# Kernel optimization log

Hardware: AMD Instinct MI355X
Metric: run time of the kernel (lower is better)

The kernel has to match this reference:

```python
import jax, jax.numpy as jnp
import numpy as np

N, C, D = 131072, 512, 3


def setup_inputs() -> dict:
    key = jax.random.key(0)
    kx, kmu = jax.random.split(key)
    X = jax.random.normal(kx, (N, D), dtype=jnp.float32)
    mu = jax.random.normal(kmu, (C, D), dtype=jnp.float32)
    w = jnp.zeros((C,), dtype=jnp.float32)
    # sigma as in __init__: r = sqrt(sum of per-dim unbiased variances of mu0)
    r = jnp.sqrt(jnp.var(mu, axis=0, ddof=1).sum())
    sigma = (0.1 * (r / C ** (1.0 / D))).astype(jnp.float32)
    return {"X": X, "mu": mu, "w": w, "sigma": sigma}


def reference(X, mu, w, sigma):
    # One EM step of a uniform-covariance GMM (EM_step_pytorch).
    n, d = X.shape
    # pairwise squared distances [N, C]
    D2_nc = ((X[:, None, :] - mu[None, :, :]) ** 2).sum(-1)
    # log-responsibilities (E-step), softmax over components
    lgamma_nc = jax.nn.log_softmax(w[None, :] - D2_nc / (2.0 * sigma ** 2), axis=1)
    gamma_nc = jnp.exp(lgamma_nc)
    # M-step: centroids (softmax over points, per component)
    mu_new = jax.nn.softmax(lgamma_nc, axis=0).T @ X  # [C, D]
    # M-step: component scores
    h_c = jax.nn.logsumexp(lgamma_nc, axis=0)  # [C]
    w_new = h_c - h_c.mean()
    # M-step: uniform std
    sigma_new = jnp.sqrt((gamma_nc * D2_nc).sum() / (d * n))
    # EM values: expected targets and free energy
    Y = gamma_nc @ mu_new  # [N, D]
    logpi_c = w_new - jax.nn.logsumexp(w_new)
    Cfe = (gamma_nc * (
        ((mu_new ** 2).sum(-1)[None, :] - (Y ** 2).sum(-1)[:, None]) / (2.0 * sigma_new ** 2)
        + d * jnp.log(sigma_new)
        - logpi_c[None, :]
        + lgamma_nc
    )).sum()
    return Y, Cfe
```

## Files before the change

### kernel.cpp

```cpp
#include <hip/hip_runtime.h>
#include <cfloat>
#include <cmath>

#define NPTS 131072
#define NC   512
#define NREP 4

#define PM4_OFF  0
#define PQ4_OFF  2048
#define ST4_OFF  4096
#define MISC_OFF 12288

__device__ __forceinline__ float waveSum(float v) {
#pragma unroll
  for (int off = 32; off > 0; off >>= 1) v += __shfl_down(v, off, 64);
  return v;
}
__device__ __forceinline__ float waveMax(float v) {
#pragma unroll
  for (int off = 32; off > 0; off >>= 1) v = fmaxf(v, __shfl_down(v, off, 64));
  return v;
}

__global__ __launch_bounds__(512) void k_prep(
    const float* __restrict__ mu, const float* __restrict__ w,
    const float* __restrict__ sigma, float4* __restrict__ pm,
    float* __restrict__ ST, float* __restrict__ misc) {
  const int t = threadIdx.x;
  const float sg = sigma[0];
  const float inv2s2 = 1.0f / (2.0f * sg * sg);
  const float m0 = mu[3 * t], m1 = mu[3 * t + 1], m2 = mu[3 * t + 2];
  pm[t] = make_float4(2.0f * inv2s2 * m0, 2.0f * inv2s2 * m1, 2.0f * inv2s2 * m2,
                      w[t] - (m0 * m0 + m1 * m1 + m2 * m2) * inv2s2);
#pragma unroll
  for (int r = 0; r < NREP * 4; ++r) ST[r * 512 + t] = 0.f;
  if (t < 8) misc[t] = 0.f;
}

__global__ __launch_bounds__(512, 8) void k_estep(
    const float* __restrict__ X, const float4* __restrict__ pm,
    float* __restrict__ ST, float* __restrict__ misc,
    float* __restrict__ out) {
  __shared__ float4 s_pt[128];
  __shared__ float2 s_ms[4][128];
  __shared__ float  s_red[8];
  __shared__ float  s_red2[8];

  const int t = threadIdx.x;
  const int p = t & 127;
  const int ch = __builtin_amdgcn_readfirstlane(t >> 7);
  const int n = blockIdx.x * 128 + p;
  const float x0 = X[3 * n], x1 = X[3 * n + 1], x2 = X[3 * n + 2];

  const float4* __restrict__ pmc = pm + ch * 128;
  float ma = -FLT_MAX, mb = -FLT_MAX, mc = -FLT_MAX, md = -FLT_MAX;
#pragma unroll 4
  for (int i = 0; i < 128; i += 4) {
    float4 a = pmc[i], b = pmc[i + 1], c = pmc[i + 2], d = pmc[i + 3];
    ma = fmaxf(ma, fmaf(a.x, x0, fmaf(a.y, x1, fmaf(a.z, x2, a.w))));
    mb = fmaxf(mb, fmaf(b.x, x0, fmaf(b.y, x1, fmaf(b.z, x2, b.w))));
    mc = fmaxf(mc, fmaf(c.x, x0, fmaf(c.y, x1, fmaf(c.z, x2, c.w))));
    md = fmaxf(md, fmaf(d.x, x0, fmaf(d.y, x1, fmaf(d.z, x2, d.w))));
  }
  const float m = fmaxf(fmaxf(ma, mb), fmaxf(mc, md));
  float sa = 0.f, sb = 0.f, sc = 0.f, sd = 0.f;
#pragma unroll 4
  for (int i = 0; i < 128; i += 4) {
    float4 a = pmc[i], b = pmc[i + 1], c = pmc[i + 2], d = pmc[i + 3];
    sa += __expf(fmaf(a.x, x0, fmaf(a.y, x1, fmaf(a.z, x2, a.w))) - m);
    sb += __expf(fmaf(b.x, x0, fmaf(b.y, x1, fmaf(b.z, x2, b.w))) - m);
    sc += __expf(fmaf(c.x, x0, fmaf(c.y, x1, fmaf(c.z, x2, c.w))) - m);
    sd += __expf(fmaf(d.x, x0, fmaf(d.y, x1, fmaf(d.z, x2, d.w))) - m);
  }
  s_ms[ch][p] = make_float2(m, (sa + sb) + (sc + sd));
  __syncthreads();

  if (t < 128) {
    float2 q0 = s_ms[0][t], q1 = s_ms[1][t], q2 = s_ms[2][t], q3 = s_ms[3][t];
    float M = fmaxf(fmaxf(q0.x, q1.x), fmaxf(q2.x, q3.x));
    float SS = q0.y * __expf(q0.x - M) + q1.y * __expf(q1.x - M) +
               q2.y * __expf(q2.x - M) + q3.y * __expf(q3.x - M);
    float z = M + __logf(SS);
    s_pt[t] = make_float4(x0, x1, x2, z);
    out[3 * n] = z;
  }
  __syncthreads();

  const float4 pc = pm[t];
  float Sg = 0.f, Tx = 0.f, Ty = 0.f, Tz = 0.f, La = 0.f;
#pragma unroll 4
  for (int i = 0; i < 128; ++i) {
    float4 pt = s_pt[i];
    float l = fmaf(pc.x, pt.x, fmaf(pc.y, pt.y, fmaf(pc.z, pt.z, pc.w)));
    float d = l - pt.w;
    float g = __expf(d);
    Sg += g;
    Tx = fmaf(g, pt.x, Tx);
    Ty = fmaf(g, pt.y, Ty);
    Tz = fmaf(g, pt.z, Tz);
    La = fmaf(g, d, La);
  }
  float* st = ST + (((blockIdx.x & (NREP - 1)) * 512 + t) << 2);
  atomicAdd(st + 0, Tx);
  atomicAdd(st + 1, Ty);
  atomicAdd(st + 2, Tz);
  atomicAdd(st + 3, Sg);

  float xx = (t < 128) ? (x0 * x0 + x1 * x1 + x2 * x2) : 0.f;
  float rx = waveSum(xx);
  float rl = waveSum(La);
  if ((t & 63) == 0) { s_red[t >> 6] = rx; s_red2[t >> 6] = rl; }
  __syncthreads();
  if (t == 0) {
    float vx = 0.f, vl = 0.f;
#pragma unroll
    for (int i = 0; i < 8; ++i) { vx += s_red[i]; vl += s_red2[i]; }
    atomicAdd(&misc[0], vx);
    atomicAdd(&misc[3], vl);
  }
}

__global__ __launch_bounds__(512) void k_mstep(
    const float* __restrict__ mu, const float4* __restrict__ ST4,
    float4* __restrict__ pq, float* __restrict__ misc,
    float* __restrict__ out) {
  __shared__ float s_red[8];
  __shared__ float s_red2[8];
  __shared__ float s_bc[4];
  const int t = threadIdx.x;

  float Tx = 0.f, Ty = 0.f, Tz = 0.f, S = 0.f;
#pragma unroll
  for (int r = 0; r < NREP; ++r) {
    float4 v = ST4[r * 512 + t];
    Tx += v.x; Ty += v.y; Tz += v.z; S += v.w;
  }
  const float Sc = fmaxf(S, 1e-30f);
  const float h = __logf(Sc);
  const float m0 = Tx / Sc, m1 = Ty / Sc, m2 = Tz / Sc;

  const float o0 = mu[3 * t], o1 = mu[3 * t + 1], o2 = mu[3 * t + 2];
  const float gdp = S * (o0 * o0 + o1 * o1 + o2 * o2)
                    - 2.0f * (o0 * Tx + o1 * Ty + o2 * Tz);

  float hm = waveMax(h);
  if ((t & 63) == 0) s_red[t >> 6] = hm;
  __syncthreads();
  if (t == 0) {
    float v = s_red[0];
    for (int i = 1; i < 8; ++i) v = fmaxf(v, s_red[i]);
    s_bc[0] = v;
  }
  __syncthreads();
  const float hM = s_bc[0];

  float es = waveSum(__expf(h - hM));
  float gs = waveSum(gdp);
  if ((t & 63) == 0) { s_red[t >> 6] = es; s_red2[t >> 6] = gs; }
  __syncthreads();
  if (t == 0) {
    float esum = 0.f, gsum = 0.f;
    for (int i = 0; i < 8; ++i) { esum += s_red[i]; gsum += s_red2[i]; }
    s_bc[1] = hM + __logf(esum);
    const float gd = fmaxf(misc[0] + gsum, 1e-20f);
    const float sn2 = gd * (1.0f / (3.0f * (float)NPTS));
    s_bc[2] = 1.0f / (2.0f * sn2);
    s_bc[3] = 1.5f * __logf(sn2);
  }
  __syncthreads();

  const float inv2s2n = s_bc[2];
  const float logpi = h - s_bc[1];
  const float A = (m0 * m0 + m1 * m1 + m2 * m2) * inv2s2n - logpi;
  pq[t] = make_float4(m0, m1, m2, A);

  float ca = waveSum(S * A);
  if ((t & 63) == 0) s_red[t >> 6] = ca;
  __syncthreads();
  if (t == 0) {
    float v = 0.f;
    for (int i = 0; i < 8; ++i) v += s_red[i];
    out[NPTS * 3] = v + misc[3] + (float)NPTS * s_bc[3];
    misc[1] = inv2s2n;
  }
}

__global__ __launch_bounds__(512, 8) void k_final(
    const float* __restrict__ X, const float4* __restrict__ pm,
    const float4* __restrict__ pq, const float* __restrict__ misc,
    float* __restrict__ out) {
  __shared__ float4 s_y[4][128];
  __shared__ float  s_red[8];

  const int t = threadIdx.x;
  const int p = t & 127;
  const int ch = __builtin_amdgcn_readfirstlane(t >> 7);
  const int n = blockIdx.x * 128 + p;
  const float x0 = X[3 * n], x1 = X[3 * n + 1], x2 = X[3 * n + 2];
  const float z = out[3 * n];
  const float inv2s2n = misc[1];

  const float4* __restrict__ pmc = pm + ch * 128;
  const float4* __restrict__ pqc = pq + ch * 128;
  float y0 = 0.f, y1 = 0.f, y2 = 0.f;
#pragma unroll 4
  for (int i = 0; i < 128; ++i) {
    float4 pp = pmc[i];
    float4 qq = pqc[i];
    float l = fmaf(pp.x, x0, fmaf(pp.y, x1, fmaf(pp.z, x2, pp.w))) - z;
    float g = __expf(l);
    y0 = fmaf(g, qq.x, y0);
    y1 = fmaf(g, qq.y, y1);
    y2 = fmaf(g, qq.z, y2);
  }
  s_y[ch][p] = make_float4(y0, y1, y2, 0.f);
  __syncthreads();

  float cfe = 0.f;
  if (t < 128) {
    float4 a0 = s_y[0][t], a1 = s_y[1][t], a2 = s_y[2][t], a3 = s_y[3][t];
    float Y0 = (a0.x + a1.x) + (a2.x + a3.x);
    float Y1 = (a0.y + a1.y) + (a2.y + a3.y);
    float Y2 = (a0.z + a1.z) + (a2.z + a3.z);
    cfe = -(Y0 * Y0 + Y1 * Y1 + Y2 * Y2) * inv2s2n;
    out[3 * n] = Y0;
    out[3 * n + 1] = Y1;
    out[3 * n + 2] = Y2;
  }
  float r = waveSum(cfe);
  if ((t & 63) == 0) s_red[t >> 6] = r;
  __syncthreads();
  if (t == 0) {
    float v = 0.f;
#pragma unroll
    for (int i = 0; i < 8; ++i) v += s_red[i];
    atomicAdd(&out[NPTS * 3], v);
  }
}

extern "C" void kernel_launch(void* const* d_in, const int* in_sizes, int n_in,
                              void* d_out, int out_size, void* d_ws, size_t ws_size,
                              hipStream_t stream) {
  const float* X = (const float*)d_in[0];
  const float* mu = (const float*)d_in[1];
  const float* w = (const float*)d_in[2];
  const float* sigma = (const float*)d_in[3];
  float* out = (float*)d_out;
  float* ws = (float*)d_ws;

  float4* pm = (float4*)(ws + PM4_OFF);
  float4* pq = (float4*)(ws + PQ4_OFF);
  float* ST = ws + ST4_OFF;
  float* misc = ws + MISC_OFF;

  k_prep<<<1, 512, 0, stream>>>(mu, w, sigma, pm, ST, misc);
  k_estep<<<NPTS / 128, 512, 0, stream>>>(X, pm, ST, misc, out);
  k_mstep<<<1, 512, 0, stream>>>(mu, (const float4*)ST, pq, misc, out);
  k_final<<<NPTS / 128, 512, 0, stream>>>(X, pm, pq, misc, out);
}
```

Baseline: 143.1 us.

## Restructure E-step in log2 domain and skip negligible responsibilities

Moves all logits into base-2 so exp2f and log2f can be used, and skips exp and accumulation work for components whose logit is more than 34 (log2 units) below the per-point max. The E-step is reorganised around 64 points per block with 8 component chunks. Logits are cached in a register array, and the entropy term is computed per point instead of per component. The point-to-component sums are scattered through LDS atomics before the global atomic flush. The final pass stages the pm/pq tables in LDS and applies the same cutoff. Gains depend on how sparse the responsibilities are. The risks are divergence, LDS atomic contention, higher register pressure, and a small approximation from dropping terms below the threshold.

```diff
diff --git a/kernel.cpp b/kernel.cpp
--- a/kernel.cpp
+++ b/kernel.cpp
@@ -5,6 +5,9 @@
 #define NPTS 131072
 #define NC   512
 #define NREP 4
+#define L2E  1.4426950408889634f
+#define LN2  0.6931471805599453f
+#define CUT  34.0f
 
 #define PM4_OFF  0
 #define PQ4_OFF  2048
@@ -28,95 +31,110 @@
     float* __restrict__ ST, float* __restrict__ misc) {
   const int t = threadIdx.x;
   const float sg = sigma[0];
-  const float inv2s2 = 1.0f / (2.0f * sg * sg);
+  const float k2 = L2E / (2.0f * sg * sg);
   const float m0 = mu[3 * t], m1 = mu[3 * t + 1], m2 = mu[3 * t + 2];
-  pm[t] = make_float4(2.0f * inv2s2 * m0, 2.0f * inv2s2 * m1, 2.0f * inv2s2 * m2,
-                      w[t] - (m0 * m0 + m1 * m1 + m2 * m2) * inv2s2);
+  pm[t] = make_float4(2.0f * k2 * m0, 2.0f * k2 * m1, 2.0f * k2 * m2,
+                      w[t] * L2E - (m0 * m0 + m1 * m1 + m2 * m2) * k2);
 #pragma unroll
   for (int r = 0; r < NREP * 4; ++r) ST[r * 512 + t] = 0.f;
   if (t < 8) misc[t] = 0.f;
 }
 
-__global__ __launch_bounds__(512, 8) void k_estep(
+__global__ __launch_bounds__(512, 4) void k_estep(
     const float* __restrict__ X, const float4* __restrict__ pm,
     float* __restrict__ ST, float* __restrict__ misc,
     float* __restrict__ out) {
-  __shared__ float4 s_pt[128];
-  __shared__ float2 s_ms[4][128];
-  __shared__ float  s_red[8];
-  __shared__ float  s_red2[8];
-
-  const int t = threadIdx.x;
-  const int p = t & 127;
-  const int ch = __builtin_amdgcn_readfirstlane(t >> 7);
-  const int n = blockIdx.x * 128 + p;
+  __shared__ float  s_m[8][64];
+  __shared__ float2 s_sq[8][64];
+  __shared__ float  s_M[64];
+  __shared__ float  s_z[64];
+  __shared__ float4 s_acc[NC];
+
+  const int t = threadIdx.x;
+  const int p = t & 63;
+  const int ch = __builtin_amdgcn_readfirstlane(t >> 6);
+  const int n = blockIdx.x * 64 + p;
   const float x0 = X[3 * n], x1 = X[3 * n + 1], x2 = X[3 * n + 2];
 
-  const float4* __restrict__ pmc = pm + ch * 128;
-  float ma = -FLT_MAX, mb = -FLT_MAX, mc = -FLT_MAX, md = -FLT_MAX;
-#pragma unroll 4
-  for (int i = 0; i < 128; i += 4) {
+  s_acc[t] = make_float4(0.f, 0.f, 0.f, 0.f);
+
+  const float4* __restrict__ pmc = pm + ch * 64;
+  float l[64];
+  float ma = -FLT_MAX, mb = -FLT_MAX, mc2 = -FLT_MAX, md = -FLT_MAX;
+#pragma unroll
+  for (int i = 0; i < 64; i += 4) {
     float4 a = pmc[i], b = pmc[i + 1], c = pmc[i + 2], d = pmc[i + 3];
-    ma = fmaxf(ma, fmaf(a.x, x0, fmaf(a.y, x1, fmaf(a.z, x2, a.w))));
-    mb = fmaxf(mb, fmaf(b.x, x0, fmaf(b.y, x1, fmaf(b.z, x2, b.w))));
-    mc = fmaxf(mc, fmaf(c.x, x0, fmaf(c.y, x1, fmaf(c.z, x2, c.w))));
-    md = fmaxf(md, fmaf(d.x, x0, fmaf(d.y, x1, fmaf(d.z, x2, d.w))));
-  }
-  const float m = fmaxf(fmaxf(ma, mb), fmaxf(mc, md));
-  float sa = 0.f, sb = 0.f, sc = 0.f, sd = 0.f;
-#pragma unroll 4
-  for (int i = 0; i < 128; i += 4) {
-    float4 a = pmc[i], b = pmc[i + 1], c = pmc[i + 2], d = pmc[i + 3];
-    sa += __expf(fmaf(a.x, x0, fmaf(a.y, x1, fmaf(a.z, x2, a.w))) - m);
-    sb += __expf(fmaf(b.x, x0, fmaf(b.y, x1, fmaf(b.z, x2, b.w))) - m);
-    sc += __expf(fmaf(c.x, x0, fmaf(c.y, x1, fmaf(c.z, x2, c.w))) - m);
-    sd += __expf(fmaf(d.x, x0, fmaf(d.y, x1, fmaf(d.z, x2, d.w))) - m);
-  }
-  s_ms[ch][p] = make_float2(m, (sa + sb) + (sc + sd));
-  __syncthreads();
-
-  if (t < 128) {
-    float2 q0 = s_ms[0][t], q1 = s_ms[1][t], q2 = s_ms[2][t], q3 = s_ms[3][t];
-    float M = fmaxf(fmaxf(q0.x, q1.x), fmaxf(q2.x, q3.x));
-    float SS = q0.y * __expf(q0.x - M) + q1.y * __expf(q1.x - M) +
-               q2.y * __expf(q2.x - M) + q3.y * __expf(q3.x - M);
-    float z = M + __logf(SS);
-    s_pt[t] = make_float4(x0, x1, x2, z);
+    l[i]     = fmaf(a.x, x0, fmaf(a.y, x1, fmaf(a.z, x2, a.w)));
+    l[i + 1] = fmaf(b.x, x0, fmaf(b.y, x1, fmaf(b.z, x2, b.w)));
+    l[i + 2] = fmaf(c.x, x0, fmaf(c.y, x1, fmaf(c.z, x2, c.w)));
+    l[i + 3] = fmaf(d.x, x0, fmaf(d.y, x1, fmaf(d.z, x2, d.w)));
+    ma  = fmaxf(ma, l[i]);      mb = fmaxf(mb, l[i + 1]);
+    mc2 = fmaxf(mc2, l[i + 2]); md = fmaxf(md, l[i + 3]);
+  }
+  s_m[ch][p] = fmaxf(fmaxf(ma, mb), fmaxf(mc2, md));
+  __syncthreads();
+
+  if (t < 64) {
+    float v = s_m[0][t];
+#pragma unroll
+    for (int c = 1; c < 8; ++c) v = fmaxf(v, s_m[c][t]);
+    s_M[t] = v;
+  }
+  __syncthreads();
+
+  const float M = s_M[p];
+  const float thr = M - CUT;
+
+  float sE = 0.f, qE = 0.f;
+#pragma unroll
+  for (int i = 0; i < 64; ++i) {
+    if (l[i] >= thr) {
+      const float d = l[i] - M;
+      const float e = exp2f(d);
+      sE += e;
+      qE = fmaf(e, d, qE);
+    }
+  }
+  s_sq[ch][p] = make_float2(sE, qE);
+  __syncthreads();
+
+  if (t < 64) {
+    float ss = 0.f, qq = 0.f;
+#pragma unroll
+    for (int c = 0; c < 8; ++c) { float2 v = s_sq[c][t]; ss += v.x; qq += v.y; }
+    const float lg = __log2f(ss);
+    const float z = s_M[t] + lg;
+    s_z[t] = z;
     out[3 * n] = z;
-  }
-  __syncthreads();
-
-  const float4 pc = pm[t];
-  float Sg = 0.f, Tx = 0.f, Ty = 0.f, Tz = 0.f, La = 0.f;
-#pragma unroll 4
-  for (int i = 0; i < 128; ++i) {
-    float4 pt = s_pt[i];
-    float l = fmaf(pc.x, pt.x, fmaf(pc.y, pt.y, fmaf(pc.z, pt.z, pc.w)));
-    float d = l - pt.w;
-    float g = __expf(d);
-    Sg += g;
-    Tx = fmaf(g, pt.x, Tx);
-    Ty = fmaf(g, pt.y, Ty);
-    Tz = fmaf(g, pt.z, Tz);
-    La = fmaf(g, d, La);
-  }
-  float* st = ST + (((blockIdx.x & (NREP - 1)) * 512 + t) << 2);
-  atomicAdd(st + 0, Tx);
-  atomicAdd(st + 1, Ty);
-  atomicAdd(st + 2, Tz);
-  atomicAdd(st + 3, Sg);
-
-  float xx = (t < 128) ? (x0 * x0 + x1 * x1 + x2 * x2) : 0.f;
-  float rx = waveSum(xx);
-  float rl = waveSum(La);
-  if ((t & 63) == 0) { s_red[t >> 6] = rx; s_red2[t >> 6] = rl; }
-  __syncthreads();
-  if (t == 0) {
-    float vx = 0.f, vl = 0.f;
-#pragma unroll
-    for (int i = 0; i < 8; ++i) { vx += s_red[i]; vl += s_red2[i]; }
-    atomicAdd(&misc[0], vx);
-    atomicAdd(&misc[3], vl);
+    const float La = LN2 * (__fdividef(qq, ss) - lg);
+    const float xx = x0 * x0 + x1 * x1 + x2 * x2;
+    const float rl = waveSum(La);
+    const float rx = waveSum(xx);
+    if (t == 0) { atomicAdd(&misc[3], rl); atomicAdd(&misc[0], rx); }
+  }
+  __syncthreads();
+
+  const float z = s_z[p];
+#pragma unroll
+  for (int i = 0; i < 64; ++i) {
+    if (l[i] >= thr) {
+      const float g = exp2f(l[i] - z);
+      float* a = (float*)(s_acc + (ch * 64 + i));
+      atomicAdd(a + 0, g * x0);
+      atomicAdd(a + 1, g * x1);
+      atomicAdd(a + 2, g * x2);
+      atomicAdd(a + 3, g);
+    }
+  }
+  __syncthreads();
+
+  float4 v = s_acc[t];
+  if (v.w != 0.f) {
+    float* st = ST + (((blockIdx.x & (NREP - 1)) * 512 + t) << 2);
+    atomicAdd(st + 0, v.x);
+    atomicAdd(st + 1, v.y);
+    atomicAdd(st + 2, v.z);
+    atomicAdd(st + 3, v.w);
   }
 }
 
@@ -185,10 +203,12 @@
   }
 }
 
-__global__ __launch_bounds__(512, 8) void k_final(
+__global__ __launch_bounds__(512, 4) void k_final(
     const float* __restrict__ X, const float4* __restrict__ pm,
     const float4* __restrict__ pq, const float* __restrict__ misc,
     float* __restrict__ out) {
+  __shared__ float4 s_pm[NC];
+  __shared__ float4 s_pq[NC];
   __shared__ float4 s_y[4][128];
   __shared__ float  s_red[8];
 
@@ -196,22 +216,30 @@
   const int p = t & 127;
   const int ch = __builtin_amdgcn_readfirstlane(t >> 7);
   const int n = blockIdx.x * 128 + p;
+
+  s_pm[t] = pm[t];
+  s_pq[t] = pq[t];
+
   const float x0 = X[3 * n], x1 = X[3 * n + 1], x2 = X[3 * n + 2];
   const float z = out[3 * n];
+  const float thr = z - CUT;
   const float inv2s2n = misc[1];
-
-  const float4* __restrict__ pmc = pm + ch * 128;
-  const float4* __restrict__ pqc = pq + ch * 128;
+  __syncthreads();
+
+  const float4* __restrict__ pmc = &s_pm[ch * 128];
+  const float4* __restrict__ pqc = &s_pq[ch * 128];
   float y0 = 0.f, y1 = 0.f, y2 = 0.f;
-#pragma unroll 4
+#pragma unroll 8
   for (int i = 0; i < 128; ++i) {
     float4 pp = pmc[i];
-    float4 qq = pqc[i];
-    float l = fmaf(pp.x, x0, fmaf(pp.y, x1, fmaf(pp.z, x2, pp.w))) - z;
-    float g = __expf(l);
-    y0 = fmaf(g, qq.x, y0);
-    y1 = fmaf(g, qq.y, y1);
-    y2 = fmaf(g, qq.z, y2);
+    const float l = fmaf(pp.x, x0, fmaf(pp.y, x1, fmaf(pp.z, x2, pp.w)));
+    if (l >= thr) {
+      const float g = exp2f(l - z);
+      float4 qq = pqc[i];
+      y0 = fmaf(g, qq.x, y0);
+      y1 = fmaf(g, qq.y, y1);
+      y2 = fmaf(g, qq.z, y2);
+    }
   }
   s_y[ch][p] = make_float4(y0, y1, y2, 0.f);
   __syncthreads();
@@ -219,9 +247,9 @@
   float cfe = 0.f;
   if (t < 128) {
     float4 a0 = s_y[0][t], a1 = s_y[1][t], a2 = s_y[2][t], a3 = s_y[3][t];
-    float Y0 = (a0.x + a1.x) + (a2.x + a3.x);
-    float Y1 = (a0.y + a1.y) + (a2.y + a3.y);
-    float Y2 = (a0.z + a1.z) + (a2.z + a3.z);
+    const float Y0 = (a0.x + a1.x) + (a2.x + a3.x);
+    const float Y1 = (a0.y + a1.y) + (a2.y + a3.y);
+    const float Y2 = (a0.z + a1.z) + (a2.z + a3.z);
     cfe = -(Y0 * Y0 + Y1 * Y1 + Y2 * Y2) * inv2s2n;
     out[3 * n] = Y0;
     out[3 * n + 1] = Y1;
@@ -254,7 +282,7 @@
   float* misc = ws + MISC_OFF;
 
   k_prep<<<1, 512, 0, stream>>>(mu, w, sigma, pm, ST, misc);
-  k_estep<<<NPTS / 128, 512, 0, stream>>>(X, pm, ST, misc, out);
+  k_estep<<<NPTS / 64, 512, 0, stream>>>(X, pm, ST, misc, out);
   k_mstep<<<1, 512, 0, stream>>>(mu, (const float4*)ST, pq, misc, out);
   k_final<<<NPTS / 128, 512, 0, stream>>>(X, pm, pq, misc, out);
 }
```

Result: slower. 175.3 us (+22.5%).

## Skip negligible responsibilities via ballot cutoff and sparse per-point component lists

Applied to the files above, without the earlier changes.

In the E-step accumulation, a wave ballot drops the exp and accumulate work when every lane's log-responsibility is below a cutoff of -34. The ballot masks are also used to build a per-point list of up to 15 significant components, which is written to workspace. The final kernel then evaluates only those listed components per point and falls back to a thresholded scan over all 512 for points that overflow the list. This trades a dense 512-component pass for sparse gathers, plus extra workspace traffic and bookkeeping. It relies on responsibilities being sharply peaked, which holds when sigma is small relative to the centroid spread.

```diff
diff --git a/kernel.cpp b/kernel.cpp
--- a/kernel.cpp
+++ b/kernel.cpp
@@ -5,11 +5,14 @@
 #define NPTS 131072
 #define NC   512
 #define NREP 4
+#define CUT  34.0f
+#define PK   15
 
 #define PM4_OFF  0
 #define PQ4_OFF  2048
 #define ST4_OFF  4096
 #define MISC_OFF 12288
+#define PL_OFF   16384
 
 __device__ __forceinline__ float waveSum(float v) {
 #pragma unroll
@@ -40,15 +43,17 @@
 __global__ __launch_bounds__(512, 8) void k_estep(
     const float* __restrict__ X, const float4* __restrict__ pm,
     float* __restrict__ ST, float* __restrict__ misc,
-    float* __restrict__ out) {
+    float* __restrict__ out, unsigned short* __restrict__ plist) {
   __shared__ float4 s_pt[128];
   __shared__ float2 s_ms[4][128];
   __shared__ float  s_red[8];
   __shared__ float  s_red2[8];
+  __shared__ unsigned long long s_hits[8][128];
 
   const int t = threadIdx.x;
   const int p = t & 127;
   const int ch = __builtin_amdgcn_readfirstlane(t >> 7);
+  const int wv = t >> 6;
   const int n = blockIdx.x * 128 + p;
   const float x0 = X[3 * n], x1 = X[3 * n + 1], x2 = X[3 * n + 2];
 
@@ -93,12 +98,16 @@
     float4 pt = s_pt[i];
     float l = fmaf(pc.x, pt.x, fmaf(pc.y, pt.y, fmaf(pc.z, pt.z, pc.w)));
     float d = l - pt.w;
-    float g = __expf(d);
-    Sg += g;
-    Tx = fmaf(g, pt.x, Tx);
-    Ty = fmaf(g, pt.y, Ty);
-    Tz = fmaf(g, pt.z, Tz);
-    La = fmaf(g, d, La);
+    const unsigned long long mask = __ballot(d >= -CUT);
+    if ((t & 63) == 0) s_hits[wv][i] = mask;
+    if (mask) {
+      float g = __expf(d);
+      Sg += g;
+      Tx = fmaf(g, pt.x, Tx);
+      Ty = fmaf(g, pt.y, Ty);
+      Tz = fmaf(g, pt.z, Tz);
+      La = fmaf(g, d, La);
+    }
   }
   float* st = ST + (((blockIdx.x & (NREP - 1)) * 512 + t) << 2);
   atomicAdd(st + 0, Tx);
@@ -117,6 +126,23 @@
     for (int i = 0; i < 8; ++i) { vx += s_red[i]; vl += s_red2[i]; }
     atomicAdd(&misc[0], vx);
     atomicAdd(&misc[3], vl);
+  }
+
+  if (plist != 0 && t < 128) {
+    unsigned short* q = plist + (size_t)n * 16u;
+    unsigned cnt = 0u;
+#pragma unroll
+    for (int w = 0; w < 8; ++w) {
+      unsigned long long hm = s_hits[w][t];
+      while (hm) {
+        const unsigned b = (unsigned)__builtin_ctzll(hm);
+        hm &= hm - 1;
+        if (cnt < (unsigned)PK) q[1 + cnt] = (unsigned short)(w * 64 + b);
+        ++cnt;
+      }
+    }
+    q[0] = (cnt > (unsigned)PK) ? (unsigned short)0xFFFFu
+                                : (unsigned short)cnt;
   }
 }
 
@@ -185,7 +211,83 @@
   }
 }
 
-__global__ __launch_bounds__(512, 8) void k_final(
+__global__ __launch_bounds__(512, 4) void k_final_list(
+    const float* __restrict__ X, const float4* __restrict__ pm,
+    const float4* __restrict__ pq, const float* __restrict__ misc,
+    float* __restrict__ out, const unsigned short* __restrict__ plist) {
+  __shared__ float4 s_pm[NC];
+  __shared__ float4 s_pq[NC];
+  __shared__ float  s_red[8];
+
+  const int t = threadIdx.x;
+  const int n = blockIdx.x * 512 + t;
+
+  s_pm[t] = pm[t];
+  s_pq[t] = pq[t];
+
+  const float x0 = X[3 * n], x1 = X[3 * n + 1], x2 = X[3 * n + 2];
+  const float z = out[3 * n];
+  const float inv2s2n = misc[1];
+
+  const uint4* __restrict__ lp =
+      reinterpret_cast<const uint4*>(plist) + ((size_t)n << 1);
+  const uint4 wA = lp[0];
+  const uint4 wB = lp[1];
+  unsigned int words[8] = {wA.x, wA.y, wA.z, wA.w, wB.x, wB.y, wB.z, wB.w};
+  const unsigned int cnt = words[0] & 0xFFFFu;
+  __syncthreads();
+
+  float y0 = 0.f, y1 = 0.f, y2 = 0.f;
+  if (cnt == 0xFFFFu) {
+    const float thr = z - CUT;
+    for (int c = 0; c < NC; ++c) {
+      float4 pp = s_pm[c];
+      const float l = fmaf(pp.x, x0, fmaf(pp.y, x1, fmaf(pp.z, x2, pp.w)));
+      if (l >= thr) {
+        const float g = __expf(l - z);
+        float4 qq = s_pq[c];
+        y0 = fmaf(g, qq.x, y0);
+        y1 = fmaf(g, qq.y, y1);
+        y2 = fmaf(g, qq.z, y2);
+      }
+    }
+  } else {
+    const int ic = (int)cnt;
+#pragma unroll
+    for (int j = 0; j < PK; ++j) {
+      if (!__any(j < ic)) break;
+      if (j < ic) {
+        const unsigned int word = words[(j + 1) >> 1];
+        const unsigned int c =
+            ((j + 1) & 1) ? (word >> 16) : (word & 0xFFFFu);
+        float4 pp = s_pm[c];
+        const float l = fmaf(pp.x, x0, fmaf(pp.y, x1, fmaf(pp.z, x2, pp.w)));
+        const float g = __expf(l - z);
+        float4 qq = s_pq[c];
+        y0 = fmaf(g, qq.x, y0);
+        y1 = fmaf(g, qq.y, y1);
+        y2 = fmaf(g, qq.z, y2);
+      }
+    }
+  }
+
+  const float cfe = -(y0 * y0 + y1 * y1 + y2 * y2) * inv2s2n;
+  out[3 * n] = y0;
+  out[3 * n + 1] = y1;
+  out[3 * n + 2] = y2;
+
+  float r = waveSum(cfe);
+  if ((t & 63) == 0) s_red[t >> 6] = r;
+  __syncthreads();
+  if (t == 0) {
+    float v = 0.f;
+#pragma unroll
+    for (int i = 0; i < 8; ++i) v += s_red[i];
+    atomicAdd(&out[NPTS * 3], v);
+  }
+}
+
+__global__ __launch_bounds__(512, 8) void k_final_dense(
     const float* __restrict__ X, const float4* __restrict__ pm,
     const float4* __restrict__ pq, const float* __restrict__ misc,
     float* __restrict__ out) {
@@ -207,8 +309,8 @@
   for (int i = 0; i < 128; ++i) {
     float4 pp = pmc[i];
     float4 qq = pqc[i];
-    float l = fmaf(pp.x, x0, fmaf(pp.y, x1, fmaf(pp.z, x2, pp.w))) - z;
-    float g = __expf(l);
+    const float l = fmaf(pp.x, x0, fmaf(pp.y, x1, fmaf(pp.z, x2, pp.w))) - z;
+    const float g = __expf(l);
     y0 = fmaf(g, qq.x, y0);
     y1 = fmaf(g, qq.y, y1);
     y2 = fmaf(g, qq.z, y2);
@@ -219,9 +321,9 @@
   float cfe = 0.f;
   if (t < 128) {
     float4 a0 = s_y[0][t], a1 = s_y[1][t], a2 = s_y[2][t], a3 = s_y[3][t];
-    float Y0 = (a0.x + a1.x) + (a2.x + a3.x);
-    float Y1 = (a0.y + a1.y) + (a2.y + a3.y);
-    float Y2 = (a0.z + a1.z) + (a2.z + a3.z);
+    const float Y0 = (a0.x + a1.x) + (a2.x + a3.x);
+    const float Y1 = (a0.y + a1.y) + (a2.y + a3.y);
+    const float Y2 = (a0.z + a1.z) + (a2.z + a3.z);
     cfe = -(Y0 * Y0 + Y1 * Y1 + Y2 * Y2) * inv2s2n;
     out[3 * n] = Y0;
     out[3 * n + 1] = Y1;
@@ -253,8 +355,15 @@
   float* ST = ws + ST4_OFF;
   float* misc = ws + MISC_OFF;
 
+  const size_t need = (size_t)PL_OFF * 4 + (size_t)NPTS * 32;
+  unsigned short* plist =
+      (ws_size >= need) ? (unsigned short*)(ws + PL_OFF) : (unsigned short*)0;
+
   k_prep<<<1, 512, 0, stream>>>(mu, w, sigma, pm, ST, misc);
-  k_estep<<<NPTS / 128, 512, 0, stream>>>(X, pm, ST, misc, out);
+  k_estep<<<NPTS / 128, 512, 0, stream>>>(X, pm, ST, misc, out, plist);
   k_mstep<<<1, 512, 0, stream>>>(mu, (const float4*)ST, pq, misc, out);
-  k_final<<<NPTS / 128, 512, 0, stream>>>(X, pm, pq, misc, out);
-}
+  if (plist)
+    k_final_list<<<NPTS / 512, 512, 0, stream>>>(X, pm, pq, misc, out, plist);
+  else
+    k_final_dense<<<NPTS / 128, 512, 0, stream>>>(X, pm, pq, misc, out);
+}
```

After: 146.4 us. 2.3% more time.

## Fuse prep, E-step, M-step and final pass into one cooperative kernel

Applied to the files above, without the earlier changes.

Replaces the four-kernel sequence with a single persistent cooperative kernel. It loops over point tiles, does a grid-wide sync, then redundantly recomputes the M-step in every block before the final Y and free-energy pass. The goal is to remove inter-kernel launch gaps and the single-block M-step launch. In exchange it adds a grid barrier, two memsets before launch, and redundant per-block prep and M-step work. The old multi-kernel path is kept as a fallback when cooperative launch is unavailable.

```diff
diff --git a/kernel.cpp b/kernel.cpp
--- a/kernel.cpp
+++ b/kernel.cpp
@@ -1,10 +1,14 @@
 #include <hip/hip_runtime.h>
+#include <hip/hip_cooperative_groups.h>
 #include <cfloat>
 #include <cmath>
+
+namespace cg = cooperative_groups;
 
 #define NPTS 131072
 #define NC   512
 #define NREP 4
+#define NT   (NPTS / 128)
 
 #define PM4_OFF  0
 #define PQ4_OFF  2048
@@ -20,6 +24,212 @@
 #pragma unroll
   for (int off = 32; off > 0; off >>= 1) v = fmaxf(v, __shfl_down(v, off, 64));
   return v;
+}
+
+__global__ __launch_bounds__(512, 8) void k_em(
+    const float* __restrict__ X, const float* __restrict__ mu,
+    const float* __restrict__ w, const float* __restrict__ sigma,
+    float4* __restrict__ pm, float4* __restrict__ pq,
+    float* __restrict__ ST, float* __restrict__ misc,
+    float* __restrict__ out) {
+  __shared__ float4 s_pt[128];
+  __shared__ float2 s_ms[4][128];
+  __shared__ float4 s_y[4][128];
+  __shared__ float  s_red[8];
+  __shared__ float  s_red2[8];
+  __shared__ float  s_bc[4];
+
+  const int t = threadIdx.x;
+  const int p = t & 127;
+  const int ch = __builtin_amdgcn_readfirstlane(t >> 7);
+  const int nblk = gridDim.x;
+
+  {
+    const float sg = sigma[0];
+    const float inv2s2 = 1.0f / (2.0f * sg * sg);
+    const float m0 = mu[3 * t], m1 = mu[3 * t + 1], m2 = mu[3 * t + 2];
+    pm[t] = make_float4(2.0f * inv2s2 * m0, 2.0f * inv2s2 * m1,
+                        2.0f * inv2s2 * m2,
+                        w[t] - (m0 * m0 + m1 * m1 + m2 * m2) * inv2s2);
+  }
+  __syncthreads();
+
+  for (int tile = blockIdx.x; tile < NT; tile += nblk) {
+    const int n = tile * 128 + p;
+    const float x0 = X[3 * n], x1 = X[3 * n + 1], x2 = X[3 * n + 2];
+
+    const float4* __restrict__ pmc = pm + ch * 128;
+    float ma = -FLT_MAX, mb = -FLT_MAX, mc = -FLT_MAX, md = -FLT_MAX;
+#pragma unroll 4
+    for (int i = 0; i < 128; i += 4) {
+      float4 a = pmc[i], b = pmc[i + 1], c = pmc[i + 2], d = pmc[i + 3];
+      ma = fmaxf(ma, fmaf(a.x, x0, fmaf(a.y, x1, fmaf(a.z, x2, a.w))));
+      mb = fmaxf(mb, fmaf(b.x, x0, fmaf(b.y, x1, fmaf(b.z, x2, b.w))));
+      mc = fmaxf(mc, fmaf(c.x, x0, fmaf(c.y, x1, fmaf(c.z, x2, c.w))));
+      md = fmaxf(md, fmaf(d.x, x0, fmaf(d.y, x1, fmaf(d.z, x2, d.w))));
+    }
+    const float m = fmaxf(fmaxf(ma, mb), fmaxf(mc, md));
+    float sa = 0.f, sb = 0.f, sc = 0.f, sd = 0.f;
+#pragma unroll 4
+    for (int i = 0; i < 128; i += 4) {
+      float4 a = pmc[i], b = pmc[i + 1], c = pmc[i + 2], d = pmc[i + 3];
+      sa += __expf(fmaf(a.x, x0, fmaf(a.y, x1, fmaf(a.z, x2, a.w))) - m);
+      sb += __expf(fmaf(b.x, x0, fmaf(b.y, x1, fmaf(b.z, x2, b.w))) - m);
+      sc += __expf(fmaf(c.x, x0, fmaf(c.y, x1, fmaf(c.z, x2, c.w))) - m);
+      sd += __expf(fmaf(d.x, x0, fmaf(d.y, x1, fmaf(d.z, x2, d.w))) - m);
+    }
+    s_ms[ch][p] = make_float2(m, (sa + sb) + (sc + sd));
+    __syncthreads();
+
+    if (t < 128) {
+      float2 q0 = s_ms[0][t], q1 = s_ms[1][t], q2 = s_ms[2][t], q3 = s_ms[3][t];
+      float M = fmaxf(fmaxf(q0.x, q1.x), fmaxf(q2.x, q3.x));
+      float SS = q0.y * __expf(q0.x - M) + q1.y * __expf(q1.x - M) +
+                 q2.y * __expf(q2.x - M) + q3.y * __expf(q3.x - M);
+      float z = M + __logf(SS);
+      s_pt[t] = make_float4(x0, x1, x2, z);
+      out[3 * n] = z;
+    }
+    __syncthreads();
+
+    const float4 pc = pm[t];
+    float Sg = 0.f, Tx = 0.f, Ty = 0.f, Tz = 0.f, La = 0.f;
+#pragma unroll 4
+    for (int i = 0; i < 128; ++i) {
+      float4 pt = s_pt[i];
+      float l = fmaf(pc.x, pt.x, fmaf(pc.y, pt.y, fmaf(pc.z, pt.z, pc.w)));
+      float d = l - pt.w;
+      float g = __expf(d);
+      Sg += g;
+      Tx = fmaf(g, pt.x, Tx);
+      Ty = fmaf(g, pt.y, Ty);
+      Tz = fmaf(g, pt.z, Tz);
+      La = fmaf(g, d, La);
+    }
+    float* st = ST + (((tile & (NREP - 1)) * 512 + t) << 2);
+    atomicAdd(st + 0, Tx);
+    atomicAdd(st + 1, Ty);
+    atomicAdd(st + 2, Tz);
+    atomicAdd(st + 3, Sg);
+
+    float xx = (t < 128) ? (x0 * x0 + x1 * x1 + x2 * x2) : 0.f;
+    float rx = waveSum(xx);
+    float rl = waveSum(La);
+    if ((t & 63) == 0) { s_red[t >> 6] = rx; s_red2[t >> 6] = rl; }
+    __syncthreads();
+    if (t == 0) {
+      float vx = 0.f, vl = 0.f;
+#pragma unroll
+      for (int i = 0; i < 8; ++i) { vx += s_red[i]; vl += s_red2[i]; }
+      atomicAdd(&misc[0], vx);
+      atomicAdd(&misc[3], vl);
+    }
+  }
+
+  __threadfence();
+  cg::this_grid().sync();
+
+  {
+    const float4* __restrict__ ST4 = (const float4*)ST;
+    float Tx = 0.f, Ty = 0.f, Tz = 0.f, S = 0.f;
+#pragma unroll
+    for (int r = 0; r < NREP; ++r) {
+      float4 v = ST4[r * 512 + t];
+      Tx += v.x; Ty += v.y; Tz += v.z; S += v.w;
+    }
+    const float Sc = fmaxf(S, 1e-30f);
+    const float h = __logf(Sc);
+    const float m0 = Tx / Sc, m1 = Ty / Sc, m2 = Tz / Sc;
+
+    const float o0 = mu[3 * t], o1 = mu[3 * t + 1], o2 = mu[3 * t + 2];
+    const float gdp = S * (o0 * o0 + o1 * o1 + o2 * o2)
+                      - 2.0f * (o0 * Tx + o1 * Ty + o2 * Tz);
+
+    float hm = waveMax(h);
+    if ((t & 63) == 0) s_red[t >> 6] = hm;
+    __syncthreads();
+    if (t == 0) {
+      float v = s_red[0];
+      for (int i = 1; i < 8; ++i) v = fmaxf(v, s_red[i]);
+      s_bc[0] = v;
+    }
+    __syncthreads();
+    const float hM = s_bc[0];
+
+    float es = waveSum(__expf(h - hM));
+    float gs = waveSum(gdp);
+    if ((t & 63) == 0) { s_red[t >> 6] = es; s_red2[t >> 6] = gs; }
+    __syncthreads();
+    if (t == 0) {
+      float esum = 0.f, gsum = 0.f;
+      for (int i = 0; i < 8; ++i) { esum += s_red[i]; gsum += s_red2[i]; }
+      s_bc[1] = hM + __logf(esum);
+      const float gd = fmaxf(misc[0] + gsum, 1e-20f);
+      const float sn2 = gd * (1.0f / (3.0f * (float)NPTS));
+      s_bc[2] = 1.0f / (2.0f * sn2);
+      s_bc[3] = 1.5f * __logf(sn2);
+    }
+    __syncthreads();
+
+    const float inv2s2n = s_bc[2];
+    const float logpi = h - s_bc[1];
+    const float A = (m0 * m0 + m1 * m1 + m2 * m2) * inv2s2n - logpi;
+    pq[t] = make_float4(m0, m1, m2, A);
+
+    float ca = waveSum(S * A);
+    if ((t & 63) == 0) s_red[t >> 6] = ca;
+    __syncthreads();
+    if (t == 0 && blockIdx.x == 0) {
+      float v = 0.f;
+      for (int i = 0; i < 8; ++i) v += s_red[i];
+      atomicAdd(&out[NPTS * 3], v + misc[3] + (float)NPTS * s_bc[3]);
+    }
+  }
+  __syncthreads();
+  const float inv2s2n = s_bc[2];
+
+  for (int tile = blockIdx.x; tile < NT; tile += nblk) {
+    const int n = tile * 128 + p;
+    const float x0 = X[3 * n], x1 = X[3 * n + 1], x2 = X[3 * n + 2];
+    const float z = out[3 * n];
+
+    const float4* __restrict__ pmc = pm + ch * 128;
+    const float4* __restrict__ pqc = pq + ch * 128;
+    float y0 = 0.f, y1 = 0.f, y2 = 0.f;
+#pragma unroll 4
+    for (int i = 0; i < 128; ++i) {
+      float4 pp = pmc[i];
+      float4 qq = pqc[i];
+      const float l = fmaf(pp.x, x0, fmaf(pp.y, x1, fmaf(pp.z, x2, pp.w))) - z;
+      const float g = __expf(l);
+      y0 = fmaf(g, qq.x, y0);
+      y1 = fmaf(g, qq.y, y1);
+      y2 = fmaf(g, qq.z, y2);
+    }
+    s_y[ch][p] = make_float4(y0, y1, y2, 0.f);
+    __syncthreads();
+
+    float cfe = 0.f;
+    if (t < 128) {
+      float4 a0 = s_y[0][t], a1 = s_y[1][t], a2 = s_y[2][t], a3 = s_y[3][t];
+      const float Y0 = (a0.x + a1.x) + (a2.x + a3.x);
+      const float Y1 = (a0.y + a1.y) + (a2.y + a3.y);
+      const float Y2 = (a0.z + a1.z) + (a2.z + a3.z);
+      cfe = -(Y0 * Y0 + Y1 * Y1 + Y2 * Y2) * inv2s2n;
+      out[3 * n] = Y0;
+      out[3 * n + 1] = Y1;
+      out[3 * n + 2] = Y2;
+    }
+    float r = waveSum(cfe);
+    if ((t & 63) == 0) s_red[t >> 6] = r;
+    __syncthreads();
+    if (t == 0) {
+      float v = 0.f;
+#pragma unroll
+      for (int i = 0; i < 8; ++i) v += s_red[i];
+      atomicAdd(&out[NPTS * 3], v);
+    }
+  }
 }
 
 __global__ __launch_bounds__(512) void k_prep(
@@ -37,7 +247,7 @@
   if (t < 8) misc[t] = 0.f;
 }
 
-__global__ __launch_bounds__(512, 8) void k_estep(
+__global__ __launch_bounds__(512, 8) void k_estep_fb(
     const float* __restrict__ X, const float4* __restrict__ pm,
     float* __restrict__ ST, float* __restrict__ misc,
     float* __restrict__ out) {
@@ -120,7 +330,7 @@
   }
 }
 
-__global__ __launch_bounds__(512) void k_mstep(
+__global__ __launch_bounds__(512) void k_mstep_fb(
     const float* __restrict__ mu, const float4* __restrict__ ST4,
     float4* __restrict__ pq, float* __restrict__ misc,
     float* __restrict__ out) {
@@ -185,7 +395,7 @@
   }
 }
 
-__global__ __launch_bounds__(512, 8) void k_final(
+__global__ __launch_bounds__(512, 8) void k_final_fb(
     const float* __restrict__ X, const float4* __restrict__ pm,
     const float4* __restrict__ pq, const float* __restrict__ misc,
     float* __restrict__ out) {
@@ -207,8 +417,8 @@
   for (int i = 0; i < 128; ++i) {
     float4 pp = pmc[i];
     float4 qq = pqc[i];
-    float l = fmaf(pp.x, x0, fmaf(pp.y, x1, fmaf(pp.z, x2, pp.w))) - z;
-    float g = __expf(l);
+    const float l = fmaf(pp.x, x0, fmaf(pp.y, x1, fmaf(pp.z, x2, pp.w))) - z;
+    const float g = __expf(l);
     y0 = fmaf(g, qq.x, y0);
     y1 = fmaf(g, qq.y, y1);
     y2 = fmaf(g, qq.z, y2);
@@ -219,9 +429,9 @@
   float cfe = 0.f;
   if (t < 128) {
     float4 a0 = s_y[0][t], a1 = s_y[1][t], a2 = s_y[2][t], a3 = s_y[3][t];
-    float Y0 = (a0.x + a1.x) + (a2.x + a3.x);
-    float Y1 = (a0.y + a1.y) + (a2.y + a3.y);
-    float Y2 = (a0.z + a1.z) + (a2.z + a3.z);
+    const float Y0 = (a0.x + a1.x) + (a2.x + a3.x);
+    const float Y1 = (a0.y + a1.y) + (a2.y + a3.y);
+    const float Y2 = (a0.z + a1.z) + (a2.z + a3.z);
     cfe = -(Y0 * Y0 + Y1 * Y1 + Y2 * Y2) * inv2s2n;
     out[3 * n] = Y0;
     out[3 * n + 1] = Y1;
@@ -253,8 +463,36 @@
   float* ST = ws + ST4_OFF;
   float* misc = ws + MISC_OFF;
 
+  static int s_grid = -1;
+  if (s_grid < 0) {
+    int dev = 0;
+    hipGetDevice(&dev);
+    int coop = 0;
+    hipDeviceGetAttribute(&coop, hipDeviceAttributeCooperativeLaunch, dev);
+    long cap = 0;
+    if (coop) {
+      int nb = 0, ncu = 0;
+      hipOccupancyMaxActiveBlocksPerMultiprocessor(&nb, k_em, 512, 0);
+      hipDeviceGetAttribute(&ncu, hipDeviceAttributeMultiprocessorCount, dev);
+      cap = (long)nb * (long)ncu;
+    }
+    s_grid = (cap >= 64) ? (int)(cap < (long)NT ? cap : (long)NT) : 0;
+  }
+
+  if (s_grid > 0) {
+    hipMemsetAsync(ST, 0, (size_t)(NREP * NC * 4 + 8) * sizeof(float), stream);
+    hipMemsetAsync(out + (size_t)NPTS * 3, 0, sizeof(float), stream);
+    void* args[] = {(void*)&X, (void*)&mu, (void*)&w, (void*)&sigma,
+                    (void*)&pm, (void*)&pq, (void*)&ST, (void*)&misc,
+                    (void*)&out};
+    hipError_t rc = hipLaunchCooperativeKernel(k_em, dim3(s_grid), dim3(512),
+                                               args, 0u, stream);
+    if (rc == hipSuccess) return;
+    s_grid = 0;
+  }
+
   k_prep<<<1, 512, 0, stream>>>(mu, w, sigma, pm, ST, misc);
-  k_estep<<<NPTS / 128, 512, 0, stream>>>(X, pm, ST, misc, out);
-  k_mstep<<<1, 512, 0, stream>>>(mu, (const float4*)ST, pq, misc, out);
-  k_final<<<NPTS / 128, 512, 0, stream>>>(X, pm, pq, misc, out);
-}
+  k_estep_fb<<<NT, 512, 0, stream>>>(X, pm, ST, misc, out);
+  k_mstep_fb<<<1, 512, 0, stream>>>(mu, (const float4*)ST, pq, misc, out);
+  k_final_fb<<<NT, 512, 0, stream>>>(X, pm, pq, misc, out);
+}
```

Measured after the change: 330.8 us. 2.31x slower.
